# Performance work log

Hardware: AMD Instinct MI355X
Metric: run time of the kernel (lower is better)

## Reference

```python
import jax, jax.numpy as jnp
import numpy as np

B, D, H = 8192, 512, 512


def _linear_init(key, out_dim, in_dim, bias=True):
    # torch nn.Linear default: U(-1/sqrt(in_dim), 1/sqrt(in_dim)) for W and b
    k1, k2 = jax.random.split(key)
    bound = 1.0 / np.sqrt(in_dim)
    W = jax.random.uniform(k1, (out_dim, in_dim), jnp.float32, -bound, bound)
    if not bias:
        return W
    b = jax.random.uniform(k2, (out_dim,), jnp.float32, -bound, bound)
    return W, b


def setup_inputs() -> dict:
    key = jax.random.key(0)
    ks = jax.random.split(key, 16)
    x = jax.random.normal(ks[0], (B, D), jnp.float32)
    delta_t = jax.random.uniform(ks[1], (B, 1), jnp.float32)
    hidden = jax.random.normal(ks[2], (B, H), jnp.float32)
    cell_s = jax.random.normal(ks[3], (B, H), jnp.float32)
    Wii, bii = _linear_init(ks[4], H, D)
    Whi, bhi = _linear_init(ks[5], H, H)
    Wig, big = _linear_init(ks[6], H, D)
    Whg, bhg = _linear_init(ks[7], H, H)
    Wio, bio = _linear_init(ks[8], H, D)
    Who, bho = _linear_init(ks[9], H, H)
    Wto, bto = _linear_init(ks[10], H, 1)
    Wco, bco = _linear_init(ks[11], H, H)
    Wit1, bit1 = _linear_init(ks[12], H, D)
    Wtt1 = _linear_init(ks[13], H, 1, bias=False)
    Wit2, bit2 = _linear_init(ks[14], H, D)
    Wtt2 = _linear_init(ks[15], H, 1, bias=False)
    return dict(x=x, delta_t=delta_t, hidden=hidden, cell_s=cell_s,
                Wii=Wii, bii=bii, Whi=Whi, bhi=bhi, Wig=Wig, big=big,
                Whg=Whg, bhg=bhg, Wio=Wio, bio=bio, Who=Who, bho=bho,
                Wto=Wto, bto=bto, Wco=Wco, bco=bco, Wit1=Wit1, bit1=bit1,
                Wtt1=Wtt1, Wit2=Wit2, bit2=bit2, Wtt2=Wtt2)


def _lin(a, W, b=None):
    y = a @ W.T
    return y if b is None else y + b


def reference(x, delta_t, hidden, cell_s,
              Wii, bii, Whi, bhi, Wig, big, Whg, bhg,
              Wio, bio, Who, bho, Wto, bto, Wco, bco,
              Wit1, bit1, Wtt1, Wit2, bit2, Wtt2):
    sig, tanh = jax.nn.sigmoid, jnp.tanh
    tm1 = sig(_lin(x, Wit1, bit1) + sig(_lin(delta_t, Wtt1)))
    tm2 = sig(_lin(x, Wit2, bit2) + sig(_lin(delta_t, Wtt2)))
    im = sig(_lin(x, Wii, bii) + _lin(hidden, Whi, bhi))
    cur_in = tanh(_lin(x, Wig, big) + _lin(hidden, Whg, bhg))
    it1 = im * tm1
    cm_t = (1.0 - it1) * cell_s + it1 * cur_in
    cm = (1.0 - im) * cell_s + im * tm2 * cur_in
    om = sig(_lin(x, Wio, bio) + _lin(delta_t, Wto, bto)
             + _lin(hidden, Who, bho) + _lin(cm_t, Wco, bco))
    hm = om * tanh(cm_t)
    return (hm, cm)
```

## Files before the change

kernel.cpp:

```cpp
#include <hip/hip_runtime.h>
#include <hip/hip_bf16.h>
#include <stdint.h>

#define B_SZ 8192
#define D_SZ 512
#define H_SZ 512
#define PRE_LD 2560

typedef __attribute__((ext_vector_type(8))) __bf16 bf16x8;
typedef __attribute__((ext_vector_type(4))) float f32x4;

__device__ __forceinline__ unsigned short f2bf(float f) {
  unsigned u = __builtin_bit_cast(unsigned, f);
  u += 0x7FFFu + ((u >> 16) & 1u);
  return (unsigned short)(u >> 16);
}
__device__ __forceinline__ float bf2f(unsigned short h) {
  unsigned u = ((unsigned)h) << 16;
  return __builtin_bit_cast(float, u);
}
__device__ __forceinline__ float sigf(float x) { return 1.0f / (1.0f + __expf(-x)); }

__device__ __forceinline__ void async_ld16(const unsigned short* g, unsigned short* l) {
  __builtin_amdgcn_global_load_lds(
      (const __attribute__((address_space(1))) unsigned int*)g,
      (__attribute__((address_space(3))) unsigned int*)l, 16, 0, 0);
}

__global__ void pack_xh(const float* __restrict__ x, const float* __restrict__ h,
                        unsigned short* __restrict__ Xb, unsigned short* __restrict__ Hb) {
  int i = (blockIdx.x * 256 + threadIdx.x) * 4;
  const float* s; unsigned short* d; int off;
  if (i < B_SZ * D_SZ) { s = x; d = Xb; off = i; }
  else                 { s = h; d = Hb; off = i - B_SZ * D_SZ; }
  float4 v = *(const float4*)(s + off);
  ushort4 o; o.x = f2bf(v.x); o.y = f2bf(v.y); o.z = f2bf(v.z); o.w = f2bf(v.w);
  *(ushort4*)(d + off) = o;
}

struct WSrcs { const float* s[9]; };

__global__ void pack_w(WSrcs ws, unsigned short* __restrict__ Wxc,
                       unsigned short* __restrict__ Whc, unsigned short* __restrict__ Wcob) {
  int i = (blockIdx.x * 256 + threadIdx.x) * 4;
  int seg = i >> 18;
  int off = i & 262143;
  const float* s = ws.s[seg] + off;
  unsigned short* d;
  if (seg < 5)      d = Wxc + (size_t)seg * 262144 + off;
  else if (seg < 8) d = Whc + (size_t)(seg - 5) * 262144 + off;
  else              d = Wcob + off;
  float4 v = *(const float4*)s;
  ushort4 o; o.x = f2bf(v.x); o.y = f2bf(v.y); o.z = f2bf(v.z); o.w = f2bf(v.w);
  *(ushort4*)d = o;
}

template <bool ACCUM>
__global__ __launch_bounds__(256, 2) void gemm_bt(
    const unsigned short* __restrict__ A, const unsigned short* __restrict__ W,
    unsigned short* __restrict__ C, int K, int ldc, int col_off) {
  __shared__ bf16x8 sA[128 * 8];
  __shared__ bf16x8 sW[128 * 8];
  const int tid  = threadIdx.x;
  const int wave = tid >> 6, lane = tid & 63;
  const int ln15 = lane & 15, kq = lane >> 4;
  const int wr = wave >> 1, wc = wave & 1;
  const long bm = (long)blockIdx.y * 128;
  const long bn = (long)blockIdx.x * 128;

  f32x4 acc[4][4];
#pragma unroll
  for (int i = 0; i < 4; ++i)
#pragma unroll
    for (int j = 0; j < 4; ++j) acc[i][j] = (f32x4){0.f, 0.f, 0.f, 0.f};

  const int nK = K >> 6;
  for (int kt = 0; kt < nK; ++kt) {
    const int k0 = kt << 6;
    __syncthreads();
#pragma unroll
    for (int it = 0; it < 4; ++it) {
      int f   = it * 256 + tid;
      int row = f >> 3;
      int col = (f & 7) << 3;
      int ldsc = it * 256 + wave * 64;
      async_ld16(A + (size_t)(bm + row) * K + k0 + col, (unsigned short*)sA + (size_t)ldsc * 8);
      async_ld16(W + (size_t)(bn + row) * K + k0 + col, (unsigned short*)sW + (size_t)ldsc * 8);
    }
    __syncthreads();
#pragma unroll
    for (int ko = 0; ko < 2; ++ko) {
      bf16x8 af[4], wf[4];
#pragma unroll
      for (int t = 0; t < 4; ++t)
        af[t] = sA[(wr * 64 + t * 16 + ln15) * 8 + ko * 4 + kq];
#pragma unroll
      for (int t = 0; t < 4; ++t)
        wf[t] = sW[(wc * 64 + t * 16 + ln15) * 8 + ko * 4 + kq];
#pragma unroll
      for (int i = 0; i < 4; ++i)
#pragma unroll
        for (int j = 0; j < 4; ++j)
          acc[i][j] = __builtin_amdgcn_mfma_f32_16x16x32_bf16(af[i], wf[j], acc[i][j], 0, 0, 0);
    }
  }
#pragma unroll
  for (int i = 0; i < 4; ++i) {
    const long r0 = bm + wr * 64 + i * 16 + kq * 4;
#pragma unroll
    for (int j = 0; j < 4; ++j) {
      const long c = bn + wc * 64 + j * 16 + ln15;
#pragma unroll
      for (int r = 0; r < 4; ++r) {
        size_t idx = (size_t)(r0 + r) * ldc + col_off + c;
        float v = acc[i][j][r];
        if (ACCUM) v += bf2f(C[idx]);
        C[idx] = f2bf(v);
      }
    }
  }
}

__global__ void gate_kernel(unsigned short* __restrict__ Pre,
                            const float* __restrict__ delta_t, const float* __restrict__ cell_s,
                            const float* __restrict__ bii, const float* __restrict__ bhi,
                            const float* __restrict__ big, const float* __restrict__ bhg,
                            const float* __restrict__ bio, const float* __restrict__ bho,
                            const float* __restrict__ Wto, const float* __restrict__ bto,
                            const float* __restrict__ bco,
                            const float* __restrict__ bit1, const float* __restrict__ Wtt1,
                            const float* __restrict__ bit2, const float* __restrict__ Wtt2,
                            float* __restrict__ out_cm, unsigned short* __restrict__ cmt_b) {
  int idx = blockIdx.x * 256 + threadIdx.x;
  int b = idx >> 9, h = idx & 511;
  size_t p = (size_t)b * PRE_LD;
  float dt = delta_t[b];
  float a1 = bf2f(Pre[p + h])        + bit1[h];
  float a2 = bf2f(Pre[p + 512 + h])  + bit2[h];
  float ai = bf2f(Pre[p + 1024 + h]) + bii[h] + bhi[h];
  float ag = bf2f(Pre[p + 1536 + h]) + big[h] + bhg[h];
  float ao = bf2f(Pre[p + 2048 + h]) + bio[h] + bho[h] + dt * Wto[h] + bto[h] + bco[h];
  float t1 = sigf(a1 + sigf(dt * Wtt1[h]));
  float t2 = sigf(a2 + sigf(dt * Wtt2[h]));
  float im = sigf(ai);
  float g  = tanhf(ag);
  float cs = cell_s[idx];
  float it1 = im * t1;
  float cmt = (1.f - it1) * cs + it1 * g;
  float cm  = (1.f - im) * cs + im * t2 * g;
  out_cm[idx] = cm;
  cmt_b[idx]  = f2bf(cmt);
  Pre[p + 2048 + h] = f2bf(ao);
}

__global__ __launch_bounds__(256, 2) void gemm_out(
    const unsigned short* __restrict__ A , const unsigned short* __restrict__ W ,
    const unsigned short* __restrict__ Pre, float* __restrict__ out_hm) {
  __shared__ bf16x8 sA[128 * 8];
  __shared__ bf16x8 sW[128 * 8];
  const int tid  = threadIdx.x;
  const int wave = tid >> 6, lane = tid & 63;
  const int ln15 = lane & 15, kq = lane >> 4;
  const int wr = wave >> 1, wc = wave & 1;
  const long bm = (long)blockIdx.y * 128;
  const long bn = (long)blockIdx.x * 128;
  const int K = H_SZ;

  f32x4 acc[4][4];
#pragma unroll
  for (int i = 0; i < 4; ++i)
#pragma unroll
    for (int j = 0; j < 4; ++j) acc[i][j] = (f32x4){0.f, 0.f, 0.f, 0.f};

  for (int kt = 0; kt < (K >> 6); ++kt) {
    const int k0 = kt << 6;
    __syncthreads();
#pragma unroll
    for (int it = 0; it < 4; ++it) {
      int f   = it * 256 + tid;
      int row = f >> 3;
      int col = (f & 7) << 3;
      int ldsc = it * 256 + wave * 64;
      async_ld16(A + (size_t)(bm + row) * K + k0 + col, (unsigned short*)sA + (size_t)ldsc * 8);
      async_ld16(W + (size_t)(bn + row) * K + k0 + col, (unsigned short*)sW + (size_t)ldsc * 8);
    }
    __syncthreads();
#pragma unroll
    for (int ko = 0; ko < 2; ++ko) {
      bf16x8 af[4], wf[4];
#pragma unroll
      for (int t = 0; t < 4; ++t)
        af[t] = sA[(wr * 64 + t * 16 + ln15) * 8 + ko * 4 + kq];
#pragma unroll
      for (int t = 0; t < 4; ++t)
        wf[t] = sW[(wc * 64 + t * 16 + ln15) * 8 + ko * 4 + kq];
#pragma unroll
      for (int i = 0; i < 4; ++i)
#pragma unroll
        for (int j = 0; j < 4; ++j)
          acc[i][j] = __builtin_amdgcn_mfma_f32_16x16x32_bf16(af[i], wf[j], acc[i][j], 0, 0, 0);
    }
  }
#pragma unroll
  for (int i = 0; i < 4; ++i) {
    const long r0 = bm + wr * 64 + i * 16 + kq * 4;
#pragma unroll
    for (int j = 0; j < 4; ++j) {
      const long c = bn + wc * 64 + j * 16 + ln15;
#pragma unroll
      for (int r = 0; r < 4; ++r) {
        long row = r0 + r;
        size_t idx = (size_t)row * H_SZ + c;
        float ao  = bf2f(Pre[(size_t)row * PRE_LD + 2048 + c]);
        float om  = sigf(ao + acc[i][j][r]);
        float cmt = bf2f(A[idx]);
        out_hm[idx] = om * tanhf(cmt);
      }
    }
  }
}

extern "C" void kernel_launch(void* const* d_in, const int* in_sizes, int n_in,
                              void* d_out, int out_size, void* d_ws, size_t ws_size,
                              hipStream_t stream) {
  const float* x    = (const float*)d_in[0];
  const float* dt   = (const float*)d_in[1];
  const float* hid  = (const float*)d_in[2];
  const float* cell = (const float*)d_in[3];
  const float* Wii  = (const float*)d_in[4];
  const float* bii  = (const float*)d_in[5];
  const float* Whi  = (const float*)d_in[6];
  const float* bhi  = (const float*)d_in[7];
  const float* Wig  = (const float*)d_in[8];
  const float* big  = (const float*)d_in[9];
  const float* Whg  = (const float*)d_in[10];
  const float* bhg  = (const float*)d_in[11];
  const float* Wio  = (const float*)d_in[12];
  const float* bio  = (const float*)d_in[13];
  const float* Who  = (const float*)d_in[14];
  const float* bho  = (const float*)d_in[15];
  const float* Wto  = (const float*)d_in[16];
  const float* bto  = (const float*)d_in[17];
  const float* Wco  = (const float*)d_in[18];
  const float* bco  = (const float*)d_in[19];
  const float* Wit1 = (const float*)d_in[20];
  const float* bit1 = (const float*)d_in[21];
  const float* Wtt1 = (const float*)d_in[22];
  const float* Wit2 = (const float*)d_in[23];
  const float* bit2 = (const float*)d_in[24];
  const float* Wtt2 = (const float*)d_in[25];

  char* wp = (char*)d_ws;
  unsigned short* Xb   = (unsigned short*)wp; wp += (size_t)B_SZ * D_SZ * 2;
  unsigned short* Hb   = (unsigned short*)wp; wp += (size_t)B_SZ * H_SZ * 2;
  unsigned short* Wxc  = (unsigned short*)wp; wp += (size_t)5 * H_SZ * D_SZ * 2;
  unsigned short* Whc  = (unsigned short*)wp; wp += (size_t)3 * H_SZ * H_SZ * 2;
  unsigned short* Wcob = (unsigned short*)wp; wp += (size_t)H_SZ * H_SZ * 2;
  unsigned short* Pre  = (unsigned short*)wp; wp += (size_t)B_SZ * PRE_LD * 2;
  unsigned short* Cmtb = (unsigned short*)wp; wp += (size_t)B_SZ * H_SZ * 2;

  float* out = (float*)d_out;

  pack_xh<<<(B_SZ * (D_SZ + H_SZ)) / 4 / 256, 256, 0, stream>>>(x, hid, Xb, Hb);
  WSrcs wsrc;
  wsrc.s[0] = Wit1; wsrc.s[1] = Wit2; wsrc.s[2] = Wii; wsrc.s[3] = Wig; wsrc.s[4] = Wio;
  wsrc.s[5] = Whi;  wsrc.s[6] = Whg;  wsrc.s[7] = Who; wsrc.s[8] = Wco;
  pack_w<<<(9 * H_SZ * D_SZ) / 4 / 256, 256, 0, stream>>>(wsrc, Wxc, Whc, Wcob);

  gemm_bt<false><<<dim3(PRE_LD / 128, B_SZ / 128), 256, 0, stream>>>(Xb, Wxc, Pre, D_SZ, PRE_LD, 0);
  gemm_bt<true><<<dim3((3 * H_SZ) / 128, B_SZ / 128), 256, 0, stream>>>(Hb, Whc, Pre, H_SZ, PRE_LD, 1024);

  gate_kernel<<<(B_SZ * H_SZ) / 256, 256, 0, stream>>>(
      Pre, dt, cell, bii, bhi, big, bhg, bio, bho, Wto, bto, bco, bit1, Wtt1, bit2, Wtt2,
      out + (size_t)B_SZ * H_SZ, Cmtb);

  gemm_out<<<dim3(H_SZ / 128, B_SZ / 128), 256, 0, stream>>>(Cmtb, Wcob, Pre, out);
}
```

Baseline: 260.7 us.

## Merge x and hidden GEMMs into one K-concatenated GEMM, vectorize gate kernel

Packs x and hidden into a single [B,1024] bf16 matrix and builds one [2560,1024] weight matrix, zero-padding the hidden half for the two time gates, so all pre-activations come from one GEMM. This removes the second launch and the read-modify-write of the Pre buffer. The gate kernel now handles four elements per thread with vector loads and stores. The cost is extra MFMA work on the zero-padded weight blocks.

New measurement: 251.6 us. 3.5% less time.

```diff
diff --git a/kernel.cpp b/kernel.cpp
--- a/kernel.cpp
+++ b/kernel.cpp
@@ -5,6 +5,8 @@
 #define B_SZ 8192
 #define D_SZ 512
 #define H_SZ 512
+#define KC 1024
+#define NPRE 2560
 #define PRE_LD 2560
 
 typedef __attribute__((ext_vector_type(8))) __bf16 bf16x8;
@@ -28,37 +30,46 @@
 }
 
 __global__ void pack_xh(const float* __restrict__ x, const float* __restrict__ h,
-                        unsigned short* __restrict__ Xb, unsigned short* __restrict__ Hb) {
+                        unsigned short* __restrict__ Ab) {
   int i = (blockIdx.x * 256 + threadIdx.x) * 4;
-  const float* s; unsigned short* d; int off;
-  if (i < B_SZ * D_SZ) { s = x; d = Xb; off = i; }
-  else                 { s = h; d = Hb; off = i - B_SZ * D_SZ; }
-  float4 v = *(const float4*)(s + off);
-  ushort4 o; o.x = f2bf(v.x); o.y = f2bf(v.y); o.z = f2bf(v.z); o.w = f2bf(v.w);
-  *(ushort4*)(d + off) = o;
-}
-
-struct WSrcs { const float* s[9]; };
-
-__global__ void pack_w(WSrcs ws, unsigned short* __restrict__ Wxc,
-                       unsigned short* __restrict__ Whc, unsigned short* __restrict__ Wcob) {
-  int i = (blockIdx.x * 256 + threadIdx.x) * 4;
-  int seg = i >> 18;
-  int off = i & 262143;
-  const float* s = ws.s[seg] + off;
-  unsigned short* d;
-  if (seg < 5)      d = Wxc + (size_t)seg * 262144 + off;
-  else if (seg < 8) d = Whc + (size_t)(seg - 5) * 262144 + off;
-  else              d = Wcob + off;
+  int b = i >> 10, c = i & 1023;
+  const float* s = (c < 512) ? (x + (size_t)b * 512 + c)
+                             : (h + (size_t)b * 512 + (c - 512));
   float4 v = *(const float4*)s;
   ushort4 o; o.x = f2bf(v.x); o.y = f2bf(v.y); o.z = f2bf(v.z); o.w = f2bf(v.w);
-  *(ushort4*)d = o;
-}
-
-template <bool ACCUM>
+  *(ushort4*)(Ab + i) = o;
+}
+
+struct WSrcs { const float* wx[5]; const float* wh[3]; const float* wco; };
+
+__global__ void pack_w(WSrcs ws, unsigned short* __restrict__ Wall,
+                       unsigned short* __restrict__ Wcob) {
+  int i = (blockIdx.x * 256 + threadIdx.x) * 4;
+  if (i < NPRE * KC) {
+    int row = i >> 10, c = i & 1023;
+    int gate = row >> 9, r = row & 511;
+    ushort4 o;
+    if (c < 512) {
+      float4 v = *(const float4*)(ws.wx[gate] + (size_t)r * 512 + c);
+      o.x = f2bf(v.x); o.y = f2bf(v.y); o.z = f2bf(v.z); o.w = f2bf(v.w);
+    } else if (gate >= 2) {
+      float4 v = *(const float4*)(ws.wh[gate - 2] + (size_t)r * 512 + (c - 512));
+      o.x = f2bf(v.x); o.y = f2bf(v.y); o.z = f2bf(v.z); o.w = f2bf(v.w);
+    } else {
+      o.x = 0; o.y = 0; o.z = 0; o.w = 0;
+    }
+    *(ushort4*)(Wall + i) = o;
+  } else {
+    int j = i - NPRE * KC;
+    float4 v = *(const float4*)(ws.wco + j);
+    ushort4 o; o.x = f2bf(v.x); o.y = f2bf(v.y); o.z = f2bf(v.z); o.w = f2bf(v.w);
+    *(ushort4*)(Wcob + j) = o;
+  }
+}
+
 __global__ __launch_bounds__(256, 2) void gemm_bt(
     const unsigned short* __restrict__ A, const unsigned short* __restrict__ W,
-    unsigned short* __restrict__ C, int K, int ldc, int col_off) {
+    unsigned short* __restrict__ C, int K, int ldc) {
   __shared__ bf16x8 sA[128 * 8];
   __shared__ bf16x8 sW[128 * 8];
   const int tid  = threadIdx.x;
@@ -111,12 +122,8 @@
     for (int j = 0; j < 4; ++j) {
       const long c = bn + wc * 64 + j * 16 + ln15;
 #pragma unroll
-      for (int r = 0; r < 4; ++r) {
-        size_t idx = (size_t)(r0 + r) * ldc + col_off + c;
-        float v = acc[i][j][r];
-        if (ACCUM) v += bf2f(C[idx]);
-        C[idx] = f2bf(v);
-      }
+      for (int r = 0; r < 4; ++r)
+        C[(size_t)(r0 + r) * ldc + c] = f2bf(acc[i][j][r]);
     }
   }
 }
@@ -131,26 +138,57 @@
                             const float* __restrict__ bit1, const float* __restrict__ Wtt1,
                             const float* __restrict__ bit2, const float* __restrict__ Wtt2,
                             float* __restrict__ out_cm, unsigned short* __restrict__ cmt_b) {
-  int idx = blockIdx.x * 256 + threadIdx.x;
-  int b = idx >> 9, h = idx & 511;
+  int i4 = (blockIdx.x * 256 + threadIdx.x) * 4;
+  int b = i4 >> 9, h = i4 & 511;
   size_t p = (size_t)b * PRE_LD;
   float dt = delta_t[b];
-  float a1 = bf2f(Pre[p + h])        + bit1[h];
-  float a2 = bf2f(Pre[p + 512 + h])  + bit2[h];
-  float ai = bf2f(Pre[p + 1024 + h]) + bii[h] + bhi[h];
-  float ag = bf2f(Pre[p + 1536 + h]) + big[h] + bhg[h];
-  float ao = bf2f(Pre[p + 2048 + h]) + bio[h] + bho[h] + dt * Wto[h] + bto[h] + bco[h];
-  float t1 = sigf(a1 + sigf(dt * Wtt1[h]));
-  float t2 = sigf(a2 + sigf(dt * Wtt2[h]));
-  float im = sigf(ai);
-  float g  = tanhf(ag);
-  float cs = cell_s[idx];
-  float it1 = im * t1;
-  float cmt = (1.f - it1) * cs + it1 * g;
-  float cm  = (1.f - im) * cs + im * t2 * g;
-  out_cm[idx] = cm;
-  cmt_b[idx]  = f2bf(cmt);
-  Pre[p + 2048 + h] = f2bf(ao);
+  ushort4 u1 = *(const ushort4*)(Pre + p + h);
+  ushort4 u2 = *(const ushort4*)(Pre + p + 512 + h);
+  ushort4 ui = *(const ushort4*)(Pre + p + 1024 + h);
+  ushort4 ug = *(const ushort4*)(Pre + p + 1536 + h);
+  ushort4 uo = *(const ushort4*)(Pre + p + 2048 + h);
+  float4 cs  = *(const float4*)(cell_s + i4);
+  float4 vbii = *(const float4*)(bii + h),  vbhi = *(const float4*)(bhi + h);
+  float4 vbig = *(const float4*)(big + h),  vbhg = *(const float4*)(bhg + h);
+  float4 vbio = *(const float4*)(bio + h),  vbho = *(const float4*)(bho + h);
+  float4 vWto = *(const float4*)(Wto + h),  vbto = *(const float4*)(bto + h);
+  float4 vbco = *(const float4*)(bco + h);
+  float4 vbt1 = *(const float4*)(bit1 + h), vwt1 = *(const float4*)(Wtt1 + h);
+  float4 vbt2 = *(const float4*)(bit2 + h), vwt2 = *(const float4*)(Wtt2 + h);
+
+  float4 ocm; ushort4 ocmt; ushort4 oao;
+  const unsigned short* pu1 = (const unsigned short*)&u1;
+  const unsigned short* pu2 = (const unsigned short*)&u2;
+  const unsigned short* pui = (const unsigned short*)&ui;
+  const unsigned short* pug = (const unsigned short*)&ug;
+  const unsigned short* puo = (const unsigned short*)&uo;
+  const float* pcs = (const float*)&cs;
+  float* pocm = (float*)&ocm;
+  unsigned short* pocmt = (unsigned short*)&ocmt;
+  unsigned short* poao = (unsigned short*)&oao;
+#pragma unroll
+  for (int l = 0; l < 4; ++l) {
+    float a1 = bf2f(pu1[l]) + ((const float*)&vbt1)[l];
+    float a2 = bf2f(pu2[l]) + ((const float*)&vbt2)[l];
+    float ai = bf2f(pui[l]) + ((const float*)&vbii)[l] + ((const float*)&vbhi)[l];
+    float ag = bf2f(pug[l]) + ((const float*)&vbig)[l] + ((const float*)&vbhg)[l];
+    float ao = bf2f(puo[l]) + ((const float*)&vbio)[l] + ((const float*)&vbho)[l]
+             + dt * ((const float*)&vWto)[l] + ((const float*)&vbto)[l] + ((const float*)&vbco)[l];
+    float t1 = sigf(a1 + sigf(dt * ((const float*)&vwt1)[l]));
+    float t2 = sigf(a2 + sigf(dt * ((const float*)&vwt2)[l]));
+    float im = sigf(ai);
+    float g  = tanhf(ag);
+    float csl = pcs[l];
+    float it1 = im * t1;
+    float cmt = (1.f - it1) * csl + it1 * g;
+    float cm  = (1.f - im) * csl + im * t2 * g;
+    pocm[l]  = cm;
+    pocmt[l] = f2bf(cmt);
+    poao[l]  = f2bf(ao);
+  }
+  *(float4*)(out_cm + i4) = ocm;
+  *(ushort4*)(cmt_b + i4) = ocmt;
+  *(ushort4*)(Pre + p + 2048 + h) = oao;
 }
 
 __global__ __launch_bounds__(256, 2) void gemm_out(
@@ -251,26 +289,23 @@
   const float* Wtt2 = (const float*)d_in[25];
 
   char* wp = (char*)d_ws;
-  unsigned short* Xb   = (unsigned short*)wp; wp += (size_t)B_SZ * D_SZ * 2;
-  unsigned short* Hb   = (unsigned short*)wp; wp += (size_t)B_SZ * H_SZ * 2;
-  unsigned short* Wxc  = (unsigned short*)wp; wp += (size_t)5 * H_SZ * D_SZ * 2;
-  unsigned short* Whc  = (unsigned short*)wp; wp += (size_t)3 * H_SZ * H_SZ * 2;
+  unsigned short* Ab   = (unsigned short*)wp; wp += (size_t)B_SZ * KC * 2;
+  unsigned short* Wall = (unsigned short*)wp; wp += (size_t)NPRE * KC * 2;
   unsigned short* Wcob = (unsigned short*)wp; wp += (size_t)H_SZ * H_SZ * 2;
   unsigned short* Pre  = (unsigned short*)wp; wp += (size_t)B_SZ * PRE_LD * 2;
   unsigned short* Cmtb = (unsigned short*)wp; wp += (size_t)B_SZ * H_SZ * 2;
 
   float* out = (float*)d_out;
 
-  pack_xh<<<(B_SZ * (D_SZ + H_SZ)) / 4 / 256, 256, 0, stream>>>(x, hid, Xb, Hb);
+  pack_xh<<<(B_SZ * KC) / 4 / 256, 256, 0, stream>>>(x, hid, Ab);
   WSrcs wsrc;
-  wsrc.s[0] = Wit1; wsrc.s[1] = Wit2; wsrc.s[2] = Wii; wsrc.s[3] = Wig; wsrc.s[4] = Wio;
-  wsrc.s[5] = Whi;  wsrc.s[6] = Whg;  wsrc.s[7] = Who; wsrc.s[8] = Wco;
-  pack_w<<<(9 * H_SZ * D_SZ) / 4 / 256, 256, 0, stream>>>(wsrc, Wxc, Whc, Wcob);
-
-  gemm_bt<false><<<dim3(PRE_LD / 128, B_SZ / 128), 256, 0, stream>>>(Xb, Wxc, Pre, D_SZ, PRE_LD, 0);
-  gemm_bt<true><<<dim3((3 * H_SZ) / 128, B_SZ / 128), 256, 0, stream>>>(Hb, Whc, Pre, H_SZ, PRE_LD, 1024);
-
-  gate_kernel<<<(B_SZ * H_SZ) / 256, 256, 0, stream>>>(
+  wsrc.wx[0] = Wit1; wsrc.wx[1] = Wit2; wsrc.wx[2] = Wii; wsrc.wx[3] = Wig; wsrc.wx[4] = Wio;
+  wsrc.wh[0] = Whi;  wsrc.wh[1] = Whg;  wsrc.wh[2] = Who; wsrc.wco = Wco;
+  pack_w<<<(NPRE * KC + H_SZ * H_SZ) / 4 / 256, 256, 0, stream>>>(wsrc, Wall, Wcob);
+
+  gemm_bt<<<dim3(NPRE / 128, B_SZ / 128), 256, 0, stream>>>(Ab, Wall, Pre, KC, PRE_LD);
+
+  gate_kernel<<<(B_SZ * H_SZ) / 4 / 256, 256, 0, stream>>>(
       Pre, dt, cell, bii, bhi, big, bhg, bio, bho, Wto, bto, bco, bit1, Wtt1, bit2, Wtt2,
       out + (size_t)B_SZ * H_SZ, Cmtb);
 
```
